# Performance work log

Hardware: AMD Instinct MI355X
Metric: run time of the kernel (lower is better)

## Reference

```python
import jax, jax.numpy as jnp
import numpy as np

N_NODES = 50000
N_EDGES = 600000
N_PAIRS = 200000
F_ATOM = 64
F_PAIR = 32
HID = 128
N_LAYERS = 3
EPS = 1e-5


def setup_inputs() -> dict:
    key = jax.random.key(0)
    ks = jax.random.split(key, 24)
    d = {}
    d["atom_features"] = jax.random.normal(ks[0], (N_NODES, F_ATOM), jnp.float32)
    d["edge_index"] = jax.random.randint(ks[1], (2, N_EDGES), 0, N_NODES)
    d["pair_indices"] = jax.random.randint(ks[2], (N_PAIRS, 2), 0, N_NODES)
    d["pair_features"] = jax.random.normal(ks[3], (N_PAIRS, F_PAIR), jnp.float32)
    # atom embedding linear
    d["embed_W"] = jax.random.normal(ks[4], (F_ATOM, HID), jnp.float32) / np.sqrt(F_ATOM)
    d["embed_b"] = jnp.zeros((HID,), jnp.float32)
    # stacked GCNConv weights [L, HID, HID]
    d["conv_W"] = jax.random.normal(ks[5], (N_LAYERS, HID, HID), jnp.float32) / np.sqrt(HID)
    d["conv_b"] = jnp.zeros((N_LAYERS, HID), jnp.float32)
    # BatchNorm (eval mode: running stats)
    d["bn_gamma"] = jnp.ones((N_LAYERS, HID), jnp.float32)
    d["bn_beta"] = jnp.zeros((N_LAYERS, HID), jnp.float32)
    d["bn_mean"] = jax.random.normal(ks[6], (N_LAYERS, HID), jnp.float32) * 0.1
    d["bn_var"] = jax.random.uniform(ks[7], (N_LAYERS, HID), jnp.float32, 0.5, 1.5)
    # pair MLP: Linear(2H+Fp -> H), Linear(H -> H//2), Linear(H//2 -> 1)
    din1 = 2 * HID + F_PAIR
    d["mlp_W1"] = jax.random.normal(ks[8], (din1, HID), jnp.float32) / np.sqrt(din1)
    d["mlp_b1"] = jnp.zeros((HID,), jnp.float32)
    d["mlp_W2"] = jax.random.normal(ks[9], (HID, HID // 2), jnp.float32) / np.sqrt(HID)
    d["mlp_b2"] = jnp.zeros((HID // 2,), jnp.float32)
    d["mlp_W3"] = jax.random.normal(ks[10], (HID // 2, 1), jnp.float32) / np.sqrt(HID // 2)
    d["mlp_b3"] = jnp.zeros((1,), jnp.float32)
    return d


def _gcn_conv(x, W, b, row, col, deg_inv_sqrt):
    # PyG GCNConv: x' = W x, then symmetric-normalized sum aggregation (self-loops
    # already folded into row/col/deg_inv_sqrt).
    h = x @ W  # [N, H]
    norm = deg_inv_sqrt[row] * deg_inv_sqrt[col]  # [E']
    msg = h[col] * norm[:, None]  # [E', H] gather
    out = jax.ops.segment_sum(msg, row, num_segments=x.shape[0])  # scatter-add
    return out + b


def reference(atom_features, edge_index, pair_indices, pair_features,
              embed_W, embed_b, conv_W, conv_b,
              bn_gamma, bn_beta, bn_mean, bn_var,
              mlp_W1, mlp_b1, mlp_W2, mlp_b2, mlp_W3, mlp_b3):
    n = atom_features.shape[0]
    # add self loops once (same for every layer)
    loop = jnp.arange(n, dtype=edge_index.dtype)
    row = jnp.concatenate([edge_index[0], loop])
    col = jnp.concatenate([edge_index[1], loop])
    deg = jax.ops.segment_sum(jnp.ones_like(row, dtype=jnp.float32), row, num_segments=n)
    deg_inv_sqrt = jnp.where(deg > 0, jax.lax.rsqrt(deg), 0.0)

    x = atom_features @ embed_W + embed_b  # [N, H]
    for i in range(N_LAYERS):
        x = _gcn_conv(x, conv_W[i], conv_b[i], row, col, deg_inv_sqrt)
        # BatchNorm1d, eval mode (running stats)
        x = (x - bn_mean[i]) * jax.lax.rsqrt(bn_var[i] + EPS) * bn_gamma[i] + bn_beta[i]
        x = jax.nn.relu(x)
        # dropout: identity in eval mode

    p0 = x[pair_indices[:, 0]]  # [P, H]
    p1 = x[pair_indices[:, 1]]  # [P, H]
    z = jnp.concatenate([p0, p1, pair_features], axis=1)  # [P, 2H+Fp]
    z = jax.nn.relu(z @ mlp_W1 + mlp_b1)
    z = jax.nn.relu(z @ mlp_W2 + mlp_b2)
    return z @ mlp_W3 + mlp_b3  # [P, 1]
```

## Files before the change

### kernel.cpp

```cpp
#include <hip/hip_runtime.h>
#include <hip/hip_bf16.h>
#include <stdint.h>

#define NN 50000
#define NE 600000
#define NP 200000
#define SCAN_CHUNK 1024
#define NB_SCAN ((NN + SCAN_CHUNK - 1) / SCAN_CHUNK)

#define PB_W    400
#define PB_CNT  ((NE + 255) / 256)
#define PB_PF   ((NP * 32 / 8 + 255) / 256)

typedef __attribute__((ext_vector_type(8))) short short8;
typedef __attribute__((ext_vector_type(4))) float f32x4;

static __device__ __forceinline__ unsigned short f2bf(float f) {
  union { float f; unsigned u; } a; a.f = f;
  unsigned r = a.u + 0x7fff + ((a.u >> 16) & 1);
  return (unsigned short)(r >> 16);
}
static __device__ __forceinline__ float bf2f(unsigned short h) {
  union { unsigned u; float f; } a; a.u = ((unsigned)h) << 16;
  return a.f;
}
static __device__ __forceinline__ float lo16f(unsigned w) {
  union { unsigned u; float f; } a; a.u = w << 16; return a.f;
}
static __device__ __forceinline__ float hi16f(unsigned w) {
  union { unsigned u; float f; } a; a.u = w & 0xffff0000u; return a.f;
}


__global__ __launch_bounds__(256) void prep_all(
    const float* __restrict__ embW, const float* __restrict__ convW,
    const float* __restrict__ W1, const float* __restrict__ W2,
    const int* __restrict__ erow, const float* __restrict__ pf,
    unsigned short* __restrict__ embT_hi, unsigned short* __restrict__ embT_lo,
    unsigned short* __restrict__ convT_hi, unsigned short* __restrict__ convT_lo,
    unsigned short* __restrict__ W1T, unsigned short* __restrict__ W2T,
    int* __restrict__ counts, unsigned short* __restrict__ pf_bf) {
  const int b = blockIdx.x, t = threadIdx.x;
  if (b < PB_W) {
    int idx = b * 256 + t;
    if (idx < 8192) {
      int n = idx >> 6, k = idx & 63;
      float v = embW[(size_t)k * 128 + n];
      unsigned short h = f2bf(v);
      embT_hi[idx] = h;
      embT_lo[idx] = f2bf(v - bf2f(h));
    } else if (idx < 8192 + 49152) {
      int i2 = idx - 8192;
      int l = i2 >> 14, n = (i2 >> 7) & 127, k = i2 & 127;
      float v = convW[(size_t)l * 16384 + (size_t)k * 128 + n];
      unsigned short h = f2bf(v);
      convT_hi[i2] = h;
      convT_lo[i2] = f2bf(v - bf2f(h));
    } else if (idx < 8192 + 49152 + 36864) {
      int i3 = idx - 57344;
      int n = i3 / 288, k = i3 % 288;
      W1T[i3] = f2bf(W1[(size_t)k * 128 + n]);
    } else if (idx < 8192 + 49152 + 36864 + 8192) {
      int i4 = idx - 94208;
      int n = i4 >> 7, k = i4 & 127;
      W2T[i4] = f2bf(W2[(size_t)k * 64 + n]);
    }
  } else if (b < PB_W + PB_CNT) {
    int e = (b - PB_W) * 256 + t;
    if (e < NE) atomicAdd(&counts[erow[e]], 1);
  } else {
    int i = (b - PB_W - PB_CNT) * 256 + t;
    if (i < NP * 32 / 8) {
      const float4* s = (const float4*)(pf + (size_t)i * 8);
      float4 v0 = s[0], v1 = s[1];
      short8 o;
      o[0] = (short)f2bf(v0.x); o[1] = (short)f2bf(v0.y);
      o[2] = (short)f2bf(v0.z); o[3] = (short)f2bf(v0.w);
      o[4] = (short)f2bf(v1.x); o[5] = (short)f2bf(v1.y);
      o[6] = (short)f2bf(v1.z); o[7] = (short)f2bf(v1.w);
      *(short8*)(pf_bf + (size_t)i * 8) = o;
    }
  }
}


__global__ __launch_bounds__(256) void scan_partial_dis(const int* __restrict__ counts,
                                                        int* __restrict__ bsum,
                                                        float* __restrict__ dis) {
  const int b = blockIdx.x, t = threadIdx.x;
  const int base = b * SCAN_CHUNK;
  int s = 0;
  for (int j = t; j < SCAN_CHUNK; j += 256) {
    int i = base + j;
    if (i < NN) {
      int cv = counts[i];
      s += cv;
      dis[i] = rsqrtf((float)cv + 1.0f);
    }
  }
  __shared__ int red[4];
#pragma unroll
  for (int off = 32; off; off >>= 1) s += __shfl_down(s, off);
  if ((t & 63) == 0) red[t >> 6] = s;
  __syncthreads();
  if (t == 0) bsum[b] = red[0] + red[1] + red[2] + red[3];
}

__global__ __launch_bounds__(256) void scan_final(const int* __restrict__ counts,
                                                  const int* __restrict__ bsum,
                                                  int* __restrict__ row_ptr,
                                                  int* __restrict__ cursor) {
  const int b = blockIdx.x, t = threadIdx.x;
  __shared__ int sb[64];
  if (t < 64) {
    int v = (t < NB_SCAN) ? bsum[t] : 0;
    int orig = v;
#pragma unroll
    for (int off = 1; off < 64; off <<= 1) {
      int u = __shfl_up(v, off);
      if (t >= off) v += u;
    }
    sb[t] = v - orig;
  }
  const int i0 = b * SCAN_CHUNK + t * 4;
  int c[4]; int s = 0;
#pragma unroll
  for (int r = 0; r < 4; ++r) { int i = i0 + r; c[r] = (i < NN) ? counts[i] : 0; s += c[r]; }
  __shared__ int sc[256];
  sc[t] = s;
  __syncthreads();
  for (int off = 1; off < 256; off <<= 1) {
    int add = (t >= off) ? sc[t - off] : 0;
    __syncthreads();
    sc[t] += add;
    __syncthreads();
  }
  int run = sb[b] + sc[t] - s;
#pragma unroll
  for (int r = 0; r < 4; ++r) {
    int i = i0 + r;
    if (i < NN) { row_ptr[i] = run; cursor[i] = run; run += c[r]; }
  }
  if (b == 0 && t == 0) row_ptr[NN] = NE;
}

__global__ void fill_kernel(const int* __restrict__ rows, const int* __restrict__ cols,
                            int* __restrict__ cursor, int* __restrict__ csr_col) {
  int e = blockIdx.x * 256 + threadIdx.x;
  if (e < NE) {
    int r = rows[e];
    int pos = atomicAdd(&cursor[r], 1);
    csr_col[pos] = cols[e];
  }
}


__global__ __launch_bounds__(256) void agg4_kernel(const unsigned short* __restrict__ xsb,
    const int* __restrict__ row_ptr, const int* __restrict__ csr_col,
    const float* __restrict__ dis, unsigned short* __restrict__ y_bf) {
  const int t = threadIdx.x;
  const int n = blockIdx.x * 4 + (t >> 6);
  if (n >= NN) return;
  const int l    = t & 63;
  const int half = l >> 5;
  const int cl   = l & 31;
  const uint2* xs2 = (const uint2*)xsb;

  float a0, a1, a2, a3;
  {
    uint2 v = make_uint2(0u, 0u);
    if (half == 0) v = xs2[(size_t)n * 32 + cl];
    a0 = lo16f(v.x); a1 = hi16f(v.x);
    a2 = lo16f(v.y); a3 = hi16f(v.y);
  }

  const int s = row_ptr[n], e = row_ptr[n + 1];
  for (int j0 = s; j0 < e; j0 += 16) {
    int idx[8];
#pragma unroll
    for (int q = 0; q < 8; ++q) {
      int j = j0 + 2 * q + half;
      idx[q] = (j < e) ? csr_col[j] : -1;
    }
    uint2 ww[8];
#pragma unroll
    for (int q = 0; q < 8; ++q) {
      int r = (idx[q] < 0) ? 0 : idx[q];
      ww[q] = xs2[(size_t)r * 32 + cl];
    }
#pragma unroll
    for (int q = 0; q < 8; ++q) {
      if (idx[q] < 0) { ww[q].x = 0u; ww[q].y = 0u; }
      a0 += lo16f(ww[q].x); a1 += hi16f(ww[q].x);
      a2 += lo16f(ww[q].y); a3 += hi16f(ww[q].y);
    }
  }

  a0 += __shfl_xor(a0, 32);
  a1 += __shfl_xor(a1, 32);
  a2 += __shfl_xor(a2, 32);
  a3 += __shfl_xor(a3, 32);

  if (half == 0) {
    float dv = dis[n];
    uint2 o;
    o.x = (unsigned)f2bf(dv * a0) | ((unsigned)f2bf(dv * a1) << 16);
    o.y = (unsigned)f2bf(dv * a2) | ((unsigned)f2bf(dv * a3) << 16);
    ((uint2*)y_bf)[(size_t)n * 32 + cl] = o;
  }
}


template<int K, int MODE, bool AF32>
__global__ __launch_bounds__(256) void mfma_gemm(
    const float* __restrict__ Af,
    const unsigned short* __restrict__ Ab,
    const unsigned short* __restrict__ BThi, const unsigned short* __restrict__ BTlo,
    const float* __restrict__ bias, const float* __restrict__ dis,
    const float* __restrict__ g, const float* __restrict__ be,
    const float* __restrict__ mn, const float* __restrict__ vr,
    unsigned short* __restrict__ outb, int M) {
  const int tid  = threadIdx.x;
  const int lane = tid & 63;
  const int w    = tid >> 6;
  const int l15  = lane & 15;
  const int khi  = (lane >> 4) * 8;
  const int rowb = blockIdx.x * 128 + w * 32;

  int ar[2];
#pragma unroll
  for (int rt = 0; rt < 2; ++rt) {
    int r = rowb + rt * 16 + l15;
    ar[rt] = (r < M) ? r : M - 1;
  }

  f32x4 acc[2][8];
#pragma unroll
  for (int rt = 0; rt < 2; ++rt)
#pragma unroll
    for (int ct = 0; ct < 8; ++ct) acc[rt][ct] = (f32x4){0.f, 0.f, 0.f, 0.f};

#pragma unroll
  for (int kb = 0; kb < K; kb += 32) {
    short8 ahi[2], alo[2];
#pragma unroll
    for (int rt = 0; rt < 2; ++rt) {
      if constexpr (AF32) {
        const float* asrc = Af + (size_t)ar[rt] * K + kb + khi;
        float4 va0 = *(const float4*)(asrc);
        float4 va1 = *(const float4*)(asrc + 4);
        float av[8] = {va0.x, va0.y, va0.z, va0.w, va1.x, va1.y, va1.z, va1.w};
#pragma unroll
        for (int j = 0; j < 8; ++j) {
          unsigned short h = f2bf(av[j]);
          ahi[rt][j] = (short)h;
          alo[rt][j] = (short)f2bf(av[j] - bf2f(h));
        }
      } else {
        ahi[rt] = *(const short8*)(Ab + (size_t)ar[rt] * K + kb + khi);
      }
    }
#pragma unroll
    for (int ct = 0; ct < 8; ++ct) {
      size_t woff = (size_t)(ct * 16 + l15) * K + kb + khi;
      short8 bhi = *(const short8*)(BThi + woff);
      short8 blo = *(const short8*)(BTlo + woff);
#pragma unroll
      for (int rt = 0; rt < 2; ++rt) {
        acc[rt][ct] = __builtin_amdgcn_mfma_f32_16x16x32_bf16(ahi[rt], bhi, acc[rt][ct], 0, 0, 0);
        if constexpr (AF32)
          acc[rt][ct] = __builtin_amdgcn_mfma_f32_16x16x32_bf16(alo[rt], bhi, acc[rt][ct], 0, 0, 0);
        acc[rt][ct] = __builtin_amdgcn_mfma_f32_16x16x32_bf16(ahi[rt], blo, acc[rt][ct], 0, 0, 0);
      }
    }
  }

#pragma unroll
  for (int rt = 0; rt < 2; ++rt) {
    const int orow0 = rowb + rt * 16 + (lane >> 4) * 4;
    float dv[4];
    if constexpr (MODE != 2) {
#pragma unroll
      for (int r = 0; r < 4; ++r) dv[r] = (orow0 + r < M) ? dis[orow0 + r] : 0.f;
    }
#pragma unroll
    for (int ct = 0; ct < 8; ++ct) {
      int col = ct * 16 + l15;
      float bb = bias[col];
      float scale = 1.f, shift = 0.f;
      if constexpr (MODE >= 1) {
        float inv = rsqrtf(vr[col] + 1e-5f);
        scale = g[col] * inv;
        shift = be[col] - mn[col] * scale;
      }
#pragma unroll
      for (int r = 0; r < 4; ++r) {
        int orow = orow0 + r;
        if (orow < M) {
          float v = acc[rt][ct][r] + bb;
          if constexpr (MODE >= 1) v = fmaxf(v * scale + shift, 0.f);
          if constexpr (MODE != 2) v *= dv[r];
          outb[(size_t)orow * 128 + col] = f2bf(v);
        }
      }
    }
  }
}


__global__ __launch_bounds__(256, 3) void mlp2_kernel(
    const unsigned short* __restrict__ xb, const int* __restrict__ pairs,
    const unsigned short* __restrict__ pfb,
    const unsigned short* __restrict__ W1T, const float* __restrict__ b1,
    const unsigned short* __restrict__ W2T, const float* __restrict__ b2,
    const float* __restrict__ W3, const float* __restrict__ b3,
    float* __restrict__ out) {
  __shared__ unsigned short H1[128 * 136];

  const int tid  = threadIdx.x;
  const int lane = tid & 63;
  const int w    = tid >> 6;
  const int pb   = blockIdx.x * 128;
  const int rowbase = w * 32;
  const int l15  = lane & 15;
  const int khi  = (lane >> 4) * 8;
  const int rq   = (lane >> 4) * 4;

  int gp0 = pb + rowbase + l15;       if (gp0 >= NP) gp0 = NP - 1;
  int gp1 = pb + rowbase + 16 + l15;  if (gp1 >= NP) gp1 = NP - 1;
  const int2 pr0 = ((const int2*)pairs)[gp0];
  const int2 pr1 = ((const int2*)pairs)[gp1];

  short8 af[18];
#pragma unroll
  for (int kb = 0; kb < 4; ++kb) {
    af[kb]     = *(const short8*)(xb + (size_t)pr0.x * 128 + kb * 32 + khi);
    af[4 + kb] = *(const short8*)(xb + (size_t)pr0.y * 128 + kb * 32 + khi);
    af[9 + kb]     = *(const short8*)(xb + (size_t)pr1.x * 128 + kb * 32 + khi);
    af[9 + 4 + kb] = *(const short8*)(xb + (size_t)pr1.y * 128 + kb * 32 + khi);
  }
  af[8]  = *(const short8*)(pfb + (size_t)gp0 * 32 + khi);
  af[17] = *(const short8*)(pfb + (size_t)gp1 * 32 + khi);

  f32x4 acc[2][8];
#pragma unroll
  for (int p = 0; p < 2; ++p)
#pragma unroll
    for (int c = 0; c < 8; ++c) acc[p][c] = (f32x4){0.f, 0.f, 0.f, 0.f};

#pragma unroll
  for (int kb = 0; kb < 9; ++kb) {
    const unsigned short* wrow = W1T + (size_t)kb * 32 + khi;
#pragma unroll
    for (int ct = 0; ct < 8; ++ct) {
      short8 bfrag = *(const short8*)(wrow + (size_t)(ct * 16 + l15) * 288);
      acc[0][ct] = __builtin_amdgcn_mfma_f32_16x16x32_bf16(af[kb], bfrag, acc[0][ct], 0, 0, 0);
      acc[1][ct] = __builtin_amdgcn_mfma_f32_16x16x32_bf16(af[9 + kb], bfrag, acc[1][ct], 0, 0, 0);
    }
  }

#pragma unroll
  for (int ct = 0; ct < 8; ++ct) {
    float bv = b1[ct * 16 + l15];
    int col = ct * 16 + l15;
#pragma unroll
    for (int p = 0; p < 2; ++p) {
#pragma unroll
      for (int r = 0; r < 4; ++r) {
        int row = rowbase + p * 16 + rq + r;
        float v = fmaxf(acc[p][ct][r] + bv, 0.f);
        H1[row * 136 + col] = f2bf(v);
      }
    }
  }
  __syncthreads();

  f32x4 acc2[2][4];
#pragma unroll
  for (int p = 0; p < 2; ++p)
#pragma unroll
    for (int c = 0; c < 4; ++c) acc2[p][c] = (f32x4){0.f, 0.f, 0.f, 0.f};

#pragma unroll
  for (int kb = 0; kb < 4; ++kb) {
    int ko = kb * 32 + khi;
    short8 a0 = *(const short8*)&H1[(rowbase + l15) * 136 + ko];
    short8 a1 = *(const short8*)&H1[(rowbase + 16 + l15) * 136 + ko];
    const unsigned short* wrow = W2T + (size_t)ko;
#pragma unroll
    for (int ct = 0; ct < 4; ++ct) {
      short8 bfrag = *(const short8*)(wrow + (size_t)(ct * 16 + l15) * 128);
      acc2[0][ct] = __builtin_amdgcn_mfma_f32_16x16x32_bf16(a0, bfrag, acc2[0][ct], 0, 0, 0);
      acc2[1][ct] = __builtin_amdgcn_mfma_f32_16x16x32_bf16(a1, bfrag, acc2[1][ct], 0, 0, 0);
    }
  }

  float w3v[4], b2v[4];
#pragma unroll
  for (int ct = 0; ct < 4; ++ct) {
    w3v[ct] = W3[ct * 16 + l15];
    b2v[ct] = b2[ct * 16 + l15];
  }
  float b3v = b3[0];
#pragma unroll
  for (int p = 0; p < 2; ++p) {
#pragma unroll
    for (int r = 0; r < 4; ++r) {
      float s = 0.f;
#pragma unroll
      for (int ct = 0; ct < 4; ++ct) {
        float h2 = fmaxf(acc2[p][ct][r] + b2v[ct], 0.f);
        s += h2 * w3v[ct];
      }
      s += __shfl_xor(s, 1);
      s += __shfl_xor(s, 2);
      s += __shfl_xor(s, 4);
      s += __shfl_xor(s, 8);
      int row = pb + rowbase + p * 16 + rq + r;
      if (l15 == 0 && row < NP) out[row] = s + b3v;
    }
  }
}


extern "C" void kernel_launch(void* const* d_in, const int* in_sizes, int n_in,
                              void* d_out, int out_size, void* d_ws, size_t ws_size,
                              hipStream_t stream) {
  (void)in_sizes; (void)n_in; (void)out_size; (void)ws_size;
  const float* atom  = (const float*)d_in[0];
  const int*   eidx  = (const int*)d_in[1];
  const int*   pairs = (const int*)d_in[2];
  const float* pfeat = (const float*)d_in[3];
  const float* embW  = (const float*)d_in[4];
  const float* embB  = (const float*)d_in[5];
  const float* convW = (const float*)d_in[6];
  const float* convB = (const float*)d_in[7];
  const float* bng   = (const float*)d_in[8];
  const float* bnb   = (const float*)d_in[9];
  const float* bnm   = (const float*)d_in[10];
  const float* bnv   = (const float*)d_in[11];
  const float* W1    = (const float*)d_in[12];
  const float* b1    = (const float*)d_in[13];
  const float* W2    = (const float*)d_in[14];
  const float* b2    = (const float*)d_in[15];
  const float* W3    = (const float*)d_in[16];
  const float* b3    = (const float*)d_in[17];
  float* out = (float*)d_out;

  uintptr_t base = (uintptr_t)d_ws;
  auto alloc = [&](size_t bytes) -> uintptr_t {
    uintptr_t p = base;
    base += (bytes + 255) & ~(size_t)255;
    return p;
  };
  int*   counts  = (int*)alloc((size_t)NN * 4);
  int*   row_ptr = (int*)alloc((size_t)(NN + 1) * 4);
  int*   cursor  = (int*)alloc((size_t)NN * 4);
  int*   csr_col = (int*)alloc((size_t)NE * 4);
  float* dis     = (float*)alloc((size_t)NN * 4);
  int*   bsum    = (int*)alloc(64 * 4);
  unsigned short* xs_bf = (unsigned short*)alloc((size_t)NN * 128 * 2);
  unsigned short* y_bf  = (unsigned short*)alloc((size_t)NN * 128 * 2);
  unsigned short* pf_bf = (unsigned short*)alloc((size_t)NP * 32 * 2);
  unsigned short* embT_hi  = (unsigned short*)alloc(8192 * 2);
  unsigned short* embT_lo  = (unsigned short*)alloc(8192 * 2);
  unsigned short* convT_hi = (unsigned short*)alloc(49152 * 2);
  unsigned short* convT_lo = (unsigned short*)alloc(49152 * 2);
  unsigned short* W1T      = (unsigned short*)alloc(36864 * 2);
  unsigned short* W2T      = (unsigned short*)alloc(8192 * 2);

  const int* erow = eidx;
  const int* ecol = eidx + NE;

  hipMemsetAsync(counts, 0, (size_t)NN * 4, stream);
  prep_all<<<PB_W + PB_CNT + PB_PF, 256, 0, stream>>>(
      embW, convW, W1, W2, erow, pfeat,
      embT_hi, embT_lo, convT_hi, convT_lo, W1T, W2T, counts, pf_bf);
  scan_partial_dis<<<NB_SCAN, 256, 0, stream>>>(counts, bsum, dis);
  scan_final<<<NB_SCAN, 256, 0, stream>>>(counts, bsum, row_ptr, cursor);
  fill_kernel<<<(NE + 255) / 256, 256, 0, stream>>>(erow, ecol, cursor, csr_col);

  mfma_gemm<64, 0, true><<<(NN + 127) / 128, 256, 0, stream>>>(
      atom, nullptr, embT_hi, embT_lo, embB, dis,
      nullptr, nullptr, nullptr, nullptr, xs_bf, NN);

  for (int l = 0; l < 3; ++l) {
    agg4_kernel<<<(NN + 3) / 4, 256, 0, stream>>>(xs_bf, row_ptr, csr_col, dis, y_bf);
    if (l < 2) {
      mfma_gemm<128, 1, false><<<(NN + 127) / 128, 256, 0, stream>>>(
          nullptr, y_bf,
          convT_hi + (size_t)l * 16384, convT_lo + (size_t)l * 16384,
          convB + (size_t)l * 128, dis,
          bng + (size_t)l * 128, bnb + (size_t)l * 128,
          bnm + (size_t)l * 128, bnv + (size_t)l * 128, xs_bf, NN);
    } else {
      mfma_gemm<128, 2, false><<<(NN + 127) / 128, 256, 0, stream>>>(
          nullptr, y_bf,
          convT_hi + (size_t)l * 16384, convT_lo + (size_t)l * 16384,
          convB + (size_t)l * 128, nullptr,
          bng + (size_t)l * 128, bnb + (size_t)l * 128,
          bnm + (size_t)l * 128, bnv + (size_t)l * 128, xs_bf, NN);
    }
  }

  mlp2_kernel<<<(NP + 127) / 128, 256, 0, stream>>>(xs_bf, pairs, pf_bf,
                                                    W1T, b1, W2T, b2, W3, b3, out);
}
```

Baseline: 334.7 us.

## Drop split-bf16 weight terms and fuse CSR fill with embedding GEMM

```diff
diff --git a/kernel.cpp b/kernel.cpp
--- a/kernel.cpp
+++ b/kernel.cpp
@@ -12,6 +12,9 @@
 #define PB_CNT  ((NE + 255) / 256)
 #define PB_PF   ((NP * 32 / 8 + 255) / 256)
 
+#define FB_FILL ((NE + 255) / 256)
+#define FB_EMB  ((NN + 127) / 128)
+
 typedef __attribute__((ext_vector_type(8))) short short8;
 typedef __attribute__((ext_vector_type(4))) float f32x4;
 
@@ -36,8 +39,7 @@
     const float* __restrict__ embW, const float* __restrict__ convW,
     const float* __restrict__ W1, const float* __restrict__ W2,
     const int* __restrict__ erow, const float* __restrict__ pf,
-    unsigned short* __restrict__ embT_hi, unsigned short* __restrict__ embT_lo,
-    unsigned short* __restrict__ convT_hi, unsigned short* __restrict__ convT_lo,
+    unsigned short* __restrict__ embT, unsigned short* __restrict__ convT,
     unsigned short* __restrict__ W1T, unsigned short* __restrict__ W2T,
     int* __restrict__ counts, unsigned short* __restrict__ pf_bf) {
   const int b = blockIdx.x, t = threadIdx.x;
@@ -45,17 +47,11 @@
     int idx = b * 256 + t;
     if (idx < 8192) {
       int n = idx >> 6, k = idx & 63;
-      float v = embW[(size_t)k * 128 + n];
-      unsigned short h = f2bf(v);
-      embT_hi[idx] = h;
-      embT_lo[idx] = f2bf(v - bf2f(h));
+      embT[idx] = f2bf(embW[(size_t)k * 128 + n]);
     } else if (idx < 8192 + 49152) {
       int i2 = idx - 8192;
       int l = i2 >> 14, n = (i2 >> 7) & 127, k = i2 & 127;
-      float v = convW[(size_t)l * 16384 + (size_t)k * 128 + n];
-      unsigned short h = f2bf(v);
-      convT_hi[i2] = h;
-      convT_lo[i2] = f2bf(v - bf2f(h));
+      convT[i2] = f2bf(convW[(size_t)l * 16384 + (size_t)k * 128 + n]);
     } else if (idx < 8192 + 49152 + 36864) {
       int i3 = idx - 57344;
       int n = i3 / 288, k = i3 % 288;
@@ -144,13 +140,91 @@
   if (b == 0 && t == 0) row_ptr[NN] = NE;
 }
 
-__global__ void fill_kernel(const int* __restrict__ rows, const int* __restrict__ cols,
-                            int* __restrict__ cursor, int* __restrict__ csr_col) {
-  int e = blockIdx.x * 256 + threadIdx.x;
-  if (e < NE) {
-    int r = rows[e];
-    int pos = atomicAdd(&cursor[r], 1);
-    csr_col[pos] = cols[e];
+
+__global__ __launch_bounds__(256) void fill_embed(
+    const int* __restrict__ erow, const int* __restrict__ ecol,
+    int* __restrict__ cursor, int* __restrict__ csr_col,
+    const float* __restrict__ atom, const unsigned short* __restrict__ embT,
+    const float* __restrict__ embB, const float* __restrict__ dis,
+    unsigned short* __restrict__ outb) {
+  const int b = blockIdx.x;
+  if (b < FB_FILL) {
+    int e = b * 256 + threadIdx.x;
+    if (e < NE) {
+      int r = erow[e];
+      int pos = atomicAdd(&cursor[r], 1);
+      csr_col[pos] = ecol[e];
+    }
+    return;
+  }
+  const int bid  = b - FB_FILL;
+  const int K    = 64;
+  const int tid  = threadIdx.x;
+  const int lane = tid & 63;
+  const int w    = tid >> 6;
+  const int l15  = lane & 15;
+  const int khi  = (lane >> 4) * 8;
+  const int rowb = bid * 128 + w * 32;
+
+  int ar[2];
+#pragma unroll
+  for (int rt = 0; rt < 2; ++rt) {
+    int r = rowb + rt * 16 + l15;
+    ar[rt] = (r < NN) ? r : NN - 1;
+  }
+
+  f32x4 acc[2][8];
+#pragma unroll
+  for (int rt = 0; rt < 2; ++rt)
+#pragma unroll
+    for (int ct = 0; ct < 8; ++ct) acc[rt][ct] = (f32x4){0.f, 0.f, 0.f, 0.f};
+
+#pragma unroll
+  for (int kb = 0; kb < K; kb += 32) {
+    short8 ahi[2], alo[2];
+#pragma unroll
+    for (int rt = 0; rt < 2; ++rt) {
+      const float* asrc = atom + (size_t)ar[rt] * K + kb + khi;
+      float4 va0 = *(const float4*)(asrc);
+      float4 va1 = *(const float4*)(asrc + 4);
+      float av[8] = {va0.x, va0.y, va0.z, va0.w, va1.x, va1.y, va1.z, va1.w};
+#pragma unroll
+      for (int j = 0; j < 8; ++j) {
+        unsigned short h = f2bf(av[j]);
+        ahi[rt][j] = (short)h;
+        alo[rt][j] = (short)f2bf(av[j] - bf2f(h));
+      }
+    }
+#pragma unroll
+    for (int ct = 0; ct < 8; ++ct) {
+      short8 bfrag = *(const short8*)(embT + (size_t)(ct * 16 + l15) * K + kb + khi);
+#pragma unroll
+      for (int rt = 0; rt < 2; ++rt) {
+        acc[rt][ct] = __builtin_amdgcn_mfma_f32_16x16x32_bf16(ahi[rt], bfrag, acc[rt][ct], 0, 0, 0);
+        acc[rt][ct] = __builtin_amdgcn_mfma_f32_16x16x32_bf16(alo[rt], bfrag, acc[rt][ct], 0, 0, 0);
+      }
+    }
+  }
+
+#pragma unroll
+  for (int rt = 0; rt < 2; ++rt) {
+    const int orow0 = rowb + rt * 16 + (lane >> 4) * 4;
+    float dv[4];
+#pragma unroll
+    for (int r = 0; r < 4; ++r) dv[r] = (orow0 + r < NN) ? dis[orow0 + r] : 0.f;
+#pragma unroll
+    for (int ct = 0; ct < 8; ++ct) {
+      int col = ct * 16 + l15;
+      float bb = embB[col];
+#pragma unroll
+      for (int r = 0; r < 4; ++r) {
+        int orow = orow0 + r;
+        if (orow < NN) {
+          float v = (acc[rt][ct][r] + bb) * dv[r];
+          outb[(size_t)orow * 128 + col] = f2bf(v);
+        }
+      }
+    }
   }
 }
 
@@ -211,15 +285,15 @@
 }
 
 
-template<int K, int MODE, bool AF32>
-__global__ __launch_bounds__(256) void mfma_gemm(
-    const float* __restrict__ Af,
+template<int MODE>
+__global__ __launch_bounds__(256) void conv_gemm(
     const unsigned short* __restrict__ Ab,
-    const unsigned short* __restrict__ BThi, const unsigned short* __restrict__ BTlo,
+    const unsigned short* __restrict__ BT,
     const float* __restrict__ bias, const float* __restrict__ dis,
     const float* __restrict__ g, const float* __restrict__ be,
     const float* __restrict__ mn, const float* __restrict__ vr,
-    unsigned short* __restrict__ outb, int M) {
+    unsigned short* __restrict__ outb) {
+  const int K    = 128;
   const int tid  = threadIdx.x;
   const int lane = tid & 63;
   const int w    = tid >> 6;
@@ -231,7 +305,7 @@
 #pragma unroll
   for (int rt = 0; rt < 2; ++rt) {
     int r = rowb + rt * 16 + l15;
-    ar[rt] = (r < M) ? r : M - 1;
+    ar[rt] = (r < NN) ? r : NN - 1;
   }
 
   f32x4 acc[2][8];
@@ -242,36 +316,16 @@
 
 #pragma unroll
   for (int kb = 0; kb < K; kb += 32) {
-    short8 ahi[2], alo[2];
-#pragma unroll
-    for (int rt = 0; rt < 2; ++rt) {
-      if constexpr (AF32) {
-        const float* asrc = Af + (size_t)ar[rt] * K + kb + khi;
-        float4 va0 = *(const float4*)(asrc);
-        float4 va1 = *(const float4*)(asrc + 4);
-        float av[8] = {va0.x, va0.y, va0.z, va0.w, va1.x, va1.y, va1.z, va1.w};
-#pragma unroll
-        for (int j = 0; j < 8; ++j) {
-          unsigned short h = f2bf(av[j]);
-          ahi[rt][j] = (short)h;
-          alo[rt][j] = (short)f2bf(av[j] - bf2f(h));
-        }
-      } else {
-        ahi[rt] = *(const short8*)(Ab + (size_t)ar[rt] * K + kb + khi);
-      }
-    }
+    short8 afr[2];
+#pragma unroll
+    for (int rt = 0; rt < 2; ++rt)
+      afr[rt] = *(const short8*)(Ab + (size_t)ar[rt] * K + kb + khi);
 #pragma unroll
     for (int ct = 0; ct < 8; ++ct) {
-      size_t woff = (size_t)(ct * 16 + l15) * K + kb + khi;
-      short8 bhi = *(const short8*)(BThi + woff);
-      short8 blo = *(const short8*)(BTlo + woff);
-#pragma unroll
-      for (int rt = 0; rt < 2; ++rt) {
-        acc[rt][ct] = __builtin_amdgcn_mfma_f32_16x16x32_bf16(ahi[rt], bhi, acc[rt][ct], 0, 0, 0);
-        if constexpr (AF32)
-          acc[rt][ct] = __builtin_amdgcn_mfma_f32_16x16x32_bf16(alo[rt], bhi, acc[rt][ct], 0, 0, 0);
-        acc[rt][ct] = __builtin_amdgcn_mfma_f32_16x16x32_bf16(ahi[rt], blo, acc[rt][ct], 0, 0, 0);
-      }
+      short8 bfrag = *(const short8*)(BT + (size_t)(ct * 16 + l15) * K + kb + khi);
+#pragma unroll
+      for (int rt = 0; rt < 2; ++rt)
+        acc[rt][ct] = __builtin_amdgcn_mfma_f32_16x16x32_bf16(afr[rt], bfrag, acc[rt][ct], 0, 0, 0);
     }
   }
 
@@ -279,27 +333,23 @@
   for (int rt = 0; rt < 2; ++rt) {
     const int orow0 = rowb + rt * 16 + (lane >> 4) * 4;
     float dv[4];
-    if constexpr (MODE != 2) {
-#pragma unroll
-      for (int r = 0; r < 4; ++r) dv[r] = (orow0 + r < M) ? dis[orow0 + r] : 0.f;
+    if constexpr (MODE == 1) {
+#pragma unroll
+      for (int r = 0; r < 4; ++r) dv[r] = (orow0 + r < NN) ? dis[orow0 + r] : 0.f;
     }
 #pragma unroll
     for (int ct = 0; ct < 8; ++ct) {
       int col = ct * 16 + l15;
       float bb = bias[col];
-      float scale = 1.f, shift = 0.f;
-      if constexpr (MODE >= 1) {
-        float inv = rsqrtf(vr[col] + 1e-5f);
-        scale = g[col] * inv;
-        shift = be[col] - mn[col] * scale;
-      }
+      float inv = rsqrtf(vr[col] + 1e-5f);
+      float scale = g[col] * inv;
+      float shift = be[col] - mn[col] * scale;
 #pragma unroll
       for (int r = 0; r < 4; ++r) {
         int orow = orow0 + r;
-        if (orow < M) {
-          float v = acc[rt][ct][r] + bb;
-          if constexpr (MODE >= 1) v = fmaxf(v * scale + shift, 0.f);
-          if constexpr (MODE != 2) v *= dv[r];
+        if (orow < NN) {
+          float v = fmaxf((acc[rt][ct][r] + bb) * scale + shift, 0.f);
+          if constexpr (MODE == 1) v *= dv[r];
           outb[(size_t)orow * 128 + col] = f2bf(v);
         }
       }
@@ -462,12 +512,10 @@
   unsigned short* xs_bf = (unsigned short*)alloc((size_t)NN * 128 * 2);
   unsigned short* y_bf  = (unsigned short*)alloc((size_t)NN * 128 * 2);
   unsigned short* pf_bf = (unsigned short*)alloc((size_t)NP * 32 * 2);
-  unsigned short* embT_hi  = (unsigned short*)alloc(8192 * 2);
-  unsigned short* embT_lo  = (unsigned short*)alloc(8192 * 2);
-  unsigned short* convT_hi = (unsigned short*)alloc(49152 * 2);
-  unsigned short* convT_lo = (unsigned short*)alloc(49152 * 2);
-  unsigned short* W1T      = (unsigned short*)alloc(36864 * 2);
-  unsigned short* W2T      = (unsigned short*)alloc(8192 * 2);
+  unsigned short* embT  = (unsigned short*)alloc(8192 * 2);
+  unsigned short* convT = (unsigned short*)alloc(49152 * 2);
+  unsigned short* W1T   = (unsigned short*)alloc(36864 * 2);
+  unsigned short* W2T   = (unsigned short*)alloc(8192 * 2);
 
   const int* erow = eidx;
   const int* ecol = eidx + NE;
@@ -475,31 +523,25 @@
   hipMemsetAsync(counts, 0, (size_t)NN * 4, stream);
   prep_all<<<PB_W + PB_CNT + PB_PF, 256, 0, stream>>>(
       embW, convW, W1, W2, erow, pfeat,
-      embT_hi, embT_lo, convT_hi, convT_lo, W1T, W2T, counts, pf_bf);
+      embT, convT, W1T, W2T, counts, pf_bf);
   scan_partial_dis<<<NB_SCAN, 256, 0, stream>>>(counts, bsum, dis);
   scan_final<<<NB_SCAN, 256, 0, stream>>>(counts, bsum, row_ptr, cursor);
-  fill_kernel<<<(NE + 255) / 256, 256, 0, stream>>>(erow, ecol, cursor, csr_col);
-
-  mfma_gemm<64, 0, true><<<(NN + 127) / 128, 256, 0, stream>>>(
-      atom, nullptr, embT_hi, embT_lo, embB, dis,
-      nullptr, nullptr, nullptr, nullptr, xs_bf, NN);
+
+  fill_embed<<<FB_FILL + FB_EMB, 256, 0, stream>>>(
+      erow, ecol, cursor, csr_col, atom, embT, embB, dis, xs_bf);
 
   for (int l = 0; l < 3; ++l) {
     agg4_kernel<<<(NN + 3) / 4, 256, 0, stream>>>(xs_bf, row_ptr, csr_col, dis, y_bf);
     if (l < 2) {
-      mfma_gemm<128, 1, false><<<(NN + 127) / 128, 256, 0, stream>>>(
-          nullptr, y_bf,
-          convT_hi + (size_t)l * 16384, convT_lo + (size_t)l * 16384,
-          convB + (size_t)l * 128, dis,
+      conv_gemm<1><<<(NN + 127) / 128, 256, 0, stream>>>(
+          y_bf, convT + (size_t)l * 16384, convB + (size_t)l * 128, dis,
           bng + (size_t)l * 128, bnb + (size_t)l * 128,
-          bnm + (size_t)l * 128, bnv + (size_t)l * 128, xs_bf, NN);
+          bnm + (size_t)l * 128, bnv + (size_t)l * 128, xs_bf);
     } else {
-      mfma_gemm<128, 2, false><<<(NN + 127) / 128, 256, 0, stream>>>(
-          nullptr, y_bf,
-          convT_hi + (size_t)l * 16384, convT_lo + (size_t)l * 16384,
-          convB + (size_t)l * 128, nullptr,
+      conv_gemm<2><<<(NN + 127) / 128, 256, 0, stream>>>(
+          y_bf, convT + (size_t)l * 16384, convB + (size_t)l * 128, nullptr,
           bng + (size_t)l * 128, bnb + (size_t)l * 128,
-          bnm + (size_t)l * 128, bnv + (size_t)l * 128, xs_bf, NN);
+          bnm + (size_t)l * 128, bnv + (size_t)l * 128, xs_bf);
     }
   }
 
```

Result: faster. 323.3 us (-3.4%).
